# Performance work log

Measured on AMD Instinct MI355X. Metric: run time of the kernel, lower is better.

## Reference

```python
import jax, jax.numpy as jnp
import numpy as np

N_GENE, N_CPG, N_MIRNA = 20000, 60000, 2000
HID, H, NL = 128, 8, 2
C = HID // H
B = 64
NEG_SLOPE = 0.2
LN_EPS = 1e-5
# edge types in HeteroConv order: (src_node_idx, dst_node_idx); node order: 0=gene,1=cpg,2=mirna
EDGE_META = [(1, 0), (0, 1), (2, 0), (0, 2), (0, 0), (0, 0), (1, 1), (2, 2)]


def layernorm(x, g, b):
    mu = jnp.mean(x, axis=-1, keepdims=True)
    var = jnp.mean(jnp.square(x - mu), axis=-1, keepdims=True)
    return (x - mu) * jax.lax.rsqrt(var + LN_EPS) * g + b


def gatv2_conv(x_src, x_dst, ei, Wl, Wr, att, bias):
    """PyG GATv2Conv, add_self_loops=False, concat heads, eval mode (no dropout)."""
    src, dst = ei[0], ei[1]
    n_dst = x_dst.shape[0]
    hs = (x_src @ Wl).reshape(-1, H, C)   # lin_l -> source features [Ns,H,C]
    hd = (x_dst @ Wr).reshape(-1, H, C)   # lin_r -> target features [Nd,H,C]
    e = jax.nn.leaky_relu(hs[src] + hd[dst], NEG_SLOPE)   # [E,H,C]
    logits = jnp.einsum('ehc,hc->eh', e, att)             # [E,H]
    # segment softmax over destination nodes
    m = jax.ops.segment_max(logits, dst, num_segments=n_dst)
    a = jnp.exp(logits - m[dst])
    s = jax.ops.segment_sum(a, dst, num_segments=n_dst)
    alpha = a / (s[dst] + 1e-16)                          # [E,H]
    msg = (hs[src] * alpha[:, :, None]).reshape(-1, HID)  # [E,HID]
    out = jax.ops.segment_sum(msg, dst, num_segments=n_dst)
    return out + bias


def setup_inputs() -> dict:
    key = jax.random.key(0)
    ks = list(jax.random.split(key, 40))
    nk = lambda: ks.pop()
    rn = lambda shape, s=0.05: jax.random.normal(nk(), shape, jnp.float32) * s

    def edges(E, Ns, Nd):
        src = jax.random.randint(nk(), (E,), 0, Ns, jnp.int32)
        dst = jax.random.randint(nk(), (E,), 0, Nd, jnp.int32)
        return jnp.stack([src, dst])

    def self_loops(N):
        ar = jnp.arange(N, dtype=jnp.int32)
        return jnp.stack([ar, ar])

    inp = {
        'batch_gene': rn((B, N_GENE), 1.0),
        'batch_meth': rn((B, N_CPG), 1.0),
        'batch_mirna': rn((B, N_MIRNA), 1.0),
        'emb_gene': rn((N_GENE, HID)),
        'emb_cpg': rn((N_CPG, HID)),
        'emb_mirna': rn((N_MIRNA, HID)),
        'Wl': rn((NL, 8, HID, HID)),
        'Wr': rn((NL, 8, HID, HID)),
        'att': rn((NL, 8, H, C)),
        'bias': rn((NL, 8, HID), 0.01),
        'ln_gamma': jnp.ones((NL, 3, HID), jnp.float32),
        'ln_beta': jnp.zeros((NL, 3, HID), jnp.float32),
        'out_gamma': jnp.ones((3, HID), jnp.float32),
        'out_beta': jnp.zeros((3, HID), jnp.float32),
        'ei_cg': edges(500000, N_CPG, N_GENE),
        'ei_gc': edges(500000, N_GENE, N_CPG),
        'ei_mg': edges(150000, N_MIRNA, N_GENE),
        'ei_gm': edges(150000, N_GENE, N_MIRNA),
        'ei_gg': edges(500000, N_GENE, N_GENE),
        'ei_sg': self_loops(N_GENE),
        'ei_sc': self_loops(N_CPG),
        'ei_sm': self_loops(N_MIRNA),
    }
    return inp


def forward(batch_gene, batch_meth, batch_mirna, emb_gene, emb_cpg, emb_mirna,
            Wl, Wr, att, bias, ln_gamma, ln_beta, out_gamma, out_beta, edge_list):
    x = [emb_gene, emb_cpg, emb_mirna]  # 0=gene,1=cpg,2=mirna
    for l in range(NL):
        agg = [jnp.zeros_like(x[0]), jnp.zeros_like(x[1]), jnp.zeros_like(x[2])]
        for t, (ei, (si, di)) in enumerate(zip(edge_list, EDGE_META)):
            agg[di] = agg[di] + gatv2_conv(x[si], x[di], ei,
                                           Wl[l, t], Wr[l, t], att[l, t], bias[l, t])
        # ELU + residual + LayerNorm per node type (dropout=0 / eval)
        x = [layernorm(x[i] + jax.nn.elu(agg[i]), ln_gamma[l, i], ln_beta[l, i])
             for i in range(3)]
    z_gene = layernorm(batch_gene @ x[0] / np.sqrt(N_GENE), out_gamma[0], out_beta[0])
    z_cpg = layernorm(batch_meth @ x[1] / np.sqrt(N_CPG), out_gamma[1], out_beta[1])
    z_mirna = layernorm(batch_mirna @ x[2] / np.sqrt(N_MIRNA), out_gamma[2], out_beta[2])
    return (z_gene, z_cpg, z_mirna)


def reference(batch_gene, batch_meth, batch_mirna, emb_gene, emb_cpg, emb_mirna,
              Wl, Wr, att, bias, ln_gamma, ln_beta, out_gamma, out_beta,
              ei_cg, ei_gc, ei_mg, ei_gm, ei_gg, ei_sg, ei_sc, ei_sm):
    edge_list = [ei_cg, ei_gc, ei_mg, ei_gm, ei_gg, ei_sg, ei_sc, ei_sm]
    return forward(batch_gene, batch_meth, batch_mirna, emb_gene, emb_cpg, emb_mirna,
                   Wl, Wr, att, bias, ln_gamma, ln_beta, out_gamma, out_beta, edge_list)
```

## Files before the change

### kernel.cpp

```cpp
#include <hip/hip_runtime.h>
#include <math.h>

typedef __attribute__((ext_vector_type(4))) float f32x4;
typedef __attribute__((ext_vector_type(2))) float f32x2;
typedef __attribute__((ext_vector_type(8))) short bf16x8;

__device__ __forceinline__ float b2f(unsigned short u) {
  return __uint_as_float(((unsigned)u) << 16);
}
__device__ __forceinline__ unsigned short f2b(float f) {
  unsigned x = __float_as_uint(f);
  unsigned r = (x + 0x7FFFu + ((x >> 16) & 1u)) >> 16;
  return (unsigned short)r;
}
__device__ __forceinline__ f32x2 bf2x2(unsigned u) {
  f32x2 r;
  r.x = __uint_as_float(u << 16);
  r.y = __uint_as_float(u & 0xFFFF0000u);
  return r;
}
__device__ __forceinline__ f32x2 pk_max(f32x2 a, f32x2 b) {
#if __has_builtin(__builtin_elementwise_max)
  return __builtin_elementwise_max(a, b);
#else
  f32x2 r; r.x = fmaxf(a.x, b.x); r.y = fmaxf(a.y, b.y); return r;
#endif
}
__device__ __forceinline__ f32x2 pk_fma(f32x2 a, f32x2 b, f32x2 c) {
#if __has_builtin(__builtin_elementwise_fma)
  return __builtin_elementwise_fma(a, b, c);
#else
  f32x2 r; r.x = fmaf(a.x, b.x, c.x); r.y = fmaf(a.y, b.y, c.y); return r;
#endif
}

#if __has_builtin(__builtin_amdgcn_cvt_pk_f32_fp8)
template<bool HI>
__device__ __forceinline__ f32x2 fp8x2_dec(unsigned w) {
  return __builtin_amdgcn_cvt_pk_f32_fp8(w, HI);
}
#else
__device__ __forceinline__ float fp8_dec1(unsigned b) {
  unsigned s = b >> 7, e = (b >> 3) & 15, m = b & 7;
  float v = (e == 0) ? (float)m * 0.001953125f
                     : __uint_as_float(((e - 7 + 127) << 23) | (m << 20));
  return s ? -v : v;
}
template<bool HI>
__device__ __forceinline__ f32x2 fp8x2_dec(unsigned w) {
  unsigned h = HI ? (w >> 16) : w;
  f32x2 r; r.x = fp8_dec1(h & 0xFF); r.y = fp8_dec1((h >> 8) & 0xFF);
  return r;
}
#endif
#if __has_builtin(__builtin_amdgcn_cvt_pk_fp8_f32)
__device__ __forceinline__ unsigned char fp8_enc_byte(float a) {
  return (unsigned char)(__builtin_amdgcn_cvt_pk_fp8_f32(a, a, 0, false) & 0xFF);
}
#else
__device__ __forceinline__ unsigned fp8_enc1(float f) {
  unsigned s = (__float_as_uint(f) >> 31) << 7;
  float a = fabsf(f);
  if (a >= 448.f) return s | 0x7E;
  if (a < 0.015625f) {
    int m = (int)(a * 512.f + 0.5f);
    return s | (unsigned)(m > 7 ? 7 : m);
  }
  int ex; (void)frexpf(a, &ex);
  int E = ex - 1;
  float sig = a * exp2f((float)(-E));
  int m = (int)((sig - 1.f) * 8.f + 0.5f);
  if (m == 8) { m = 0; E += 1; }
  if (E > 8) return s | 0x7E;
  return s | (unsigned)((E + 7) << 3) | (unsigned)m;
}
__device__ __forceinline__ unsigned char fp8_enc_byte(float a) {
  return (unsigned char)fp8_enc1(a);
}
#endif

__global__ __launch_bounds__(256) void prep_w(
    const float* __restrict__ Wl, const float* __restrict__ Wr,
    unsigned short* __restrict__ wt)
{
  int elem = blockIdx.x * 256 + threadIdx.x;
  int mat = elem >> 14;
  int c = (elem >> 7) & 127;
  int k = elem & 127;
  const float* srcb = (mat & 1) ? Wr : Wl;
  wt[elem] = f2b(srcb[((long)(mat >> 1) << 14) + (k << 7) + c]);
}

__global__ __launch_bounds__(256) void cast_all(
    const float* __restrict__ e0, const float* __restrict__ e1,
    const float* __restrict__ e2, unsigned short* __restrict__ x0,
    unsigned short* __restrict__ x1, unsigned short* __restrict__ x2,
    int n0, int n1, int n2)
{
  int i = blockIdx.x * 256 + threadIdx.x;
  const float* s; unsigned short* d; int loc = i;
  if (loc < n0) { s = e0; d = x0; }
  else {
    loc -= n0;
    if (loc < n1) { s = e1; d = x1; }
    else { loc -= n1; if (loc >= n2) return; s = e2; d = x2; }
  }
  float4 v = *(const float4*)(s + (long)loc * 4);
  ushort4 o = {f2b(v.x), f2b(v.y), f2b(v.z), f2b(v.w)};
  *(ushort4*)(d + (long)loc * 4) = o;
}

__global__ __launch_bounds__(128) void prep_bias(
    const float* __restrict__ bias, float* __restrict__ bsum)
{
  int c = threadIdx.x;
  const int TM[3] = {0x35, 0x42, 0x88};
  for (int l = 0; l < 2; ++l)
    for (int ty = 0; ty < 3; ++ty) {
      float s = 0.f;
      for (int t = 0; t < 8; ++t)
        if (TM[ty] & (1 << t)) s += bias[(l * 8 + t) * 128 + c];
      bsum[(l * 3 + ty) * 128 + c] = s;
    }
}

struct MPJob {
  const unsigned short* x; int N; int nw;
  const unsigned short* wt[4]; void* out[4]; int mode[4];
};
struct MPArgs { MPJob j[4]; int off[5]; };

__global__ __launch_bounds__(256) void mproj_multi(MPArgs a)
{
  __shared__ __align__(16) char lx[32768];
  __shared__ __align__(16) char lw[32768];
  int blk = blockIdx.x, t = 0;
  while (blk >= a.off[t + 1]) ++t;
  const MPJob& J = a.j[t];
  const long r0 = (long)(blk - a.off[t]) * 128;
  const int tid = threadIdx.x;
  const int N = J.N;

#pragma unroll
  for (int i = 0; i < 8; ++i) {
    int ch = i * 256 + tid;
    int row = ch >> 4, k0 = (ch & 15) << 3;
    uint4 xv = {0u, 0u, 0u, 0u};
    if (r0 + row < N) xv = *(const uint4*)(J.x + (r0 + row) * 128 + k0);
    *(uint4*)(lx + ((row * 256 + k0 * 2) ^ ((row & 7) << 4))) = xv;
  }

  const int lane = tid & 63;
  const int lr = lane & 15, lk = lane >> 4;
  const int rbase = (tid >> 6) * 32;

  for (int w = 0; w < J.nw; ++w) {
    __syncthreads();
    const unsigned short* wt = J.wt[w];
#pragma unroll
    for (int i = 0; i < 8; ++i) {
      int ch = i * 256 + tid;
      int row = ch >> 4;
      uint4 wv = *(const uint4*)(wt + (long)ch * 8);
      *(uint4*)(lw + ((ch * 16) ^ ((row & 7) << 4))) = wv;
    }
    __syncthreads();

    f32x4 acc[2][8] = {};
#pragma unroll
    for (int kb = 0; kb < 4; ++kb) {
      int k = kb * 32 + lk * 8;
      int ra = rbase + lr;
      bf16x8 a0 = *(const bf16x8*)(lx + ((ra * 256 + k * 2) ^ ((ra & 7) << 4)));
      int rb = rbase + 16 + lr;
      bf16x8 a1 = *(const bf16x8*)(lx + ((rb * 256 + k * 2) ^ ((rb & 7) << 4)));
#pragma unroll
      for (int cc = 0; cc < 8; ++cc) {
        int col = cc * 16 + lr;
        bf16x8 bfr = *(const bf16x8*)(lw + ((col * 256 + k * 2) ^ ((col & 7) << 4)));
        acc[0][cc] = __builtin_amdgcn_mfma_f32_16x16x32_bf16(a0, bfr, acc[0][cc], 0, 0, 0);
        acc[1][cc] = __builtin_amdgcn_mfma_f32_16x16x32_bf16(a1, bfr, acc[1][cc], 0, 0, 0);
      }
    }
    int mode = J.mode[w];
    void* outv = J.out[w];
#pragma unroll
    for (int rt = 0; rt < 2; ++rt) {
      int rowb = rbase + rt * 16 + lk * 4;
#pragma unroll
      for (int cc = 0; cc < 8; ++cc) {
        int col = cc * 16 + lr;
#pragma unroll
        for (int q = 0; q < 4; ++q) {
          long row = r0 + rowb + q;
          if (row < N) {
            if (mode == 3)
              ((unsigned char*)outv)[row * 128 + col] = fp8_enc_byte(acc[rt][cc][q]);
            else if (mode == 2)
              ((unsigned short*)outv)[row * 128 + col] = f2b(acc[rt][cc][q]);
            else
              ((float*)outv)[row * 128 + col] = acc[rt][cc][q];
          }
        }
      }
    }
  }
}

struct BArgs {
  const int* src[5]; const int* dst[5];
  int* cnt[5];
  int* tmp[5];
  int* rs[5];
  int* csrc[5];
  int E[5], Nd[5], NB[5], B[5];
  int cOff[6], fOff[6];
};

__global__ __launch_bounds__(256) void bucket_count(BArgs a)
{
  __shared__ int h[512];
  int blk = blockIdx.x, t = 0;
  while (blk >= a.cOff[t + 1]) ++t;
  int lb = blk - a.cOff[t];
  int B = a.B[t], NB = a.NB[t], E = a.E[t];
  for (int i = threadIdx.x; i < B; i += 256) h[i] = 0;
  __syncthreads();
  const int* dst = a.dst[t];
  int base = lb * 4096;
#pragma unroll
  for (int j = 0; j < 16; ++j) {
    int e = base + j * 256 + threadIdx.x;
    if (e < E) atomicAdd(&h[dst[e] >> 7], 1);
  }
  __syncthreads();
  int* cnt = a.cnt[t];
  for (int b = threadIdx.x; b < B; b += 256) cnt[b * NB + lb] = h[b];
}

__global__ __launch_bounds__(1024) void bucket_scan(BArgs a)
{
  int t = blockIdx.x;
  int n = a.B[t] * a.NB[t];
  int* dp = a.cnt[t];
  __shared__ int wsum[16];
  __shared__ int sbase, ctot;
  int tid = threadIdx.x;
  int lane = tid & 63, wid = tid >> 6;
  if (tid == 0) sbase = 0;
  __syncthreads();
  for (int chunk = 0; chunk < n; chunk += 16384) {
    int idx0 = chunk + tid * 16;
    int v[16], lsum = 0;
#pragma unroll
    for (int j = 0; j < 16; ++j) {
      v[j] = (idx0 + j < n) ? dp[idx0 + j] : 0;
      lsum += v[j];
    }
    int sc = lsum;
#pragma unroll
    for (int o = 1; o < 64; o <<= 1) {
      int u = __shfl_up(sc, o);
      if (lane >= o) sc += u;
    }
    if (lane == 63) wsum[wid] = sc;
    __syncthreads();
    if (wid == 0) {
      int w = (lane < 16) ? wsum[lane] : 0;
      int s2 = w;
#pragma unroll
      for (int o = 1; o < 16; o <<= 1) {
        int u = __shfl_up(s2, o);
        if (lane >= o) s2 += u;
      }
      if (lane < 16) wsum[lane] = s2 - w;
      if (lane == 15) ctot = s2;
    }
    __syncthreads();
    int excl = sbase + wsum[wid] + (sc - lsum);
#pragma unroll
    for (int j = 0; j < 16; ++j) {
      if (idx0 + j < n) dp[idx0 + j] = excl;
      excl += v[j];
    }
    __syncthreads();
    if (tid == 0) sbase += ctot;
    __syncthreads();
  }
}

__global__ __launch_bounds__(256) void bucket_scatter(BArgs a)
{
  __shared__ int cur[512];
  int blk = blockIdx.x, t = 0;
  while (blk >= a.cOff[t + 1]) ++t;
  int lb = blk - a.cOff[t];
  int B = a.B[t], NB = a.NB[t], E = a.E[t];
  const int* cnt = a.cnt[t];
  for (int b = threadIdx.x; b < B; b += 256) cur[b] = cnt[b * NB + lb];
  __syncthreads();
  const int* src = a.src[t];
  const int* dst = a.dst[t];
  int* tmp = a.tmp[t];
  int base = lb * 4096;
#pragma unroll
  for (int j = 0; j < 16; ++j) {
    int e = base + j * 256 + threadIdx.x;
    if (e < E) {
      int dv = dst[e];
      int pos = atomicAdd(&cur[dv >> 7], 1);
      tmp[pos] = ((dv & 127) << 16) | src[e];
    }
  }
}

__global__ __launch_bounds__(256) void bucket_finalize(BArgs a)
{
  __shared__ int h[128], sc[128], ex[128], cur[128];
  int blk = blockIdx.x, t = 0;
  while (blk >= a.fOff[t + 1]) ++t;
  int b = blk - a.fOff[t];
  int B = a.B[t], NB = a.NB[t], E = a.E[t], Nd = a.Nd[t];
  const int* cnt = a.cnt[t];
  const int* tmp = a.tmp[t];
  int* rs = a.rs[t];
  int* csrc = a.csrc[t];
  int tid = threadIdx.x;
  int beg = cnt[b * NB];
  int end = (b + 1 < B) ? cnt[(b + 1) * NB] : E;
  if (tid < 128) h[tid] = 0;
  __syncthreads();
  for (int i = beg + tid; i < end; i += 256)
    atomicAdd(&h[tmp[i] >> 16], 1);
  __syncthreads();
  if (tid < 128) sc[tid] = h[tid];
  __syncthreads();
#pragma unroll
  for (int off = 1; off < 128; off <<= 1) {
    int v = (tid < 128 && tid >= off) ? sc[tid - off] : 0;
    __syncthreads();
    if (tid < 128) sc[tid] += v;
    __syncthreads();
  }
  if (tid < 128) {
    ex[tid] = sc[tid] - h[tid];
    cur[tid] = 0;
    int dg = b * 128 + tid;
    if (dg < Nd) rs[dg] = beg + ex[tid];
  }
  if (b == B - 1 && tid == 0) rs[Nd] = E;
  __syncthreads();
  for (int i = beg + tid; i < end; i += 256) {
    int v = tmp[i];
    int d = v >> 16;
    int r = atomicAdd(&cur[d], 1);
    csrc[beg + ex[d] + r] = v & 0xFFFF;
  }
}

struct GSeg {
  const int* rs[3]; const int* csrc[3];
  const unsigned char* hs[3]; const unsigned short* hd[3];
  const float* att[3];
  const float* aggSelf;
  const float* xin;
  float* xf; unsigned short* xb;
  const float* bsum;
  const float* gam; const float* bet;
  int Nd; int ntypes;
};
struct GArgs { GSeg s[3]; int off[4]; };

__global__ __launch_bounds__(256) void gat_gather_ln(GArgs g)
{
  int blk = blockIdx.x, si = 0;
  while (blk >= g.off[si + 1]) ++si;
  const GSeg& sg = g.s[si];
  int d = (blk - g.off[si]) * 4 + (threadIdx.x >> 6);
  if (d >= sg.Nd) return;
  int lane = threadIdx.x & 63;
  int q = lane >> 4, j = lane & 15;
  f32x2 T0 = {0.f, 0.f}, T1 = {0.f, 0.f}, T2 = {0.f, 0.f}, T3 = {0.f, 0.f};
  for (int k = 0; k < sg.ntypes; ++k) {
    const float* ap = sg.att[k] + 8 * j;
    float4 aa = *(const float4*)ap;
    float4 ab = *(const float4*)(ap + 4);
    f32x2 A0 = {aa.x, aa.y}, A1 = {aa.z, aa.w};
    f32x2 A2 = {ab.x, ab.y}, A3 = {ab.z, ab.w};
    uint4 hu = *((const uint4*)(sg.hd[k] + (long)d * 128) + j);
    f32x2 H0 = bf2x2(hu.x), H1 = bf2x2(hu.y);
    f32x2 H2 = bf2x2(hu.z), H3 = bf2x2(hu.w);
    const int* cs = sg.csrc[k];
    const unsigned char* hsk = sg.hs[k];
    int beg = sg.rs[k][d], end = sg.rs[k][d + 1];
    f32x2 n0 = {0.f, 0.f}, n1 = {0.f, 0.f}, n2 = {0.f, 0.f}, n3 = {0.f, 0.f};
    float D = 0.f;

#define GA_EDGE(U)                                                          \
    {                                                                       \
      f32x2 h0 = fp8x2_dec<false>((U).x), h1 = fp8x2_dec<true>((U).x);      \
      f32x2 h2 = fp8x2_dec<false>((U).y), h3 = fp8x2_dec<true>((U).y);      \
      f32x2 v0 = h0 + H0, v1 = h1 + H1, v2 = h2 + H2, v3 = h3 + H3;         \
      v0 = pk_max(v0, v0 * 0.2f);                                           \
      v1 = pk_max(v1, v1 * 0.2f);                                           \
      v2 = pk_max(v2, v2 * 0.2f);                                           \
      v3 = pk_max(v3, v3 * 0.2f);                                           \
      f32x2 pv = pk_fma(v0, A0, pk_fma(v1, A1, pk_fma(v2, A2, v3 * A3)));   \
      float p = pv.x + pv.y;                                                \
      p += __shfl_xor(p, 1);                                                \
      float a = __expf(fminf(p, 60.f));                                     \
      f32x2 av = {a, a};                                                    \
      n0 = pk_fma(h0, av, n0);                                              \
      n1 = pk_fma(h1, av, n1);                                              \
      n2 = pk_fma(h2, av, n2);                                              \
      n3 = pk_fma(h3, av, n3);                                              \
      D += a;                                                               \
    }

    int i = beg + q;
    int sA = (i < end) ? cs[i] : 0;
    int sB = (i + 4 < end) ? cs[i + 4] : 0;
    for (; i + 4 < end; i += 8) {
      uint2 u0 = *((const uint2*)(hsk + (long)sA * 128) + j);
      uint2 u1 = *((const uint2*)(hsk + (long)sB * 128) + j);
      sA = (i + 8 < end) ? cs[i + 8] : 0;
      sB = (i + 12 < end) ? cs[i + 12] : 0;
      GA_EDGE(u0);
      GA_EDGE(u1);
    }
    if (i < end) {
      uint2 u = *((const uint2*)(hsk + (long)sA * 128) + j);
      GA_EDGE(u);
    }
#undef GA_EDGE

#pragma unroll
    for (int o = 16; o < 64; o <<= 1) {
      n0.x += __shfl_xor(n0.x, o); n0.y += __shfl_xor(n0.y, o);
      n1.x += __shfl_xor(n1.x, o); n1.y += __shfl_xor(n1.y, o);
      n2.x += __shfl_xor(n2.x, o); n2.y += __shfl_xor(n2.y, o);
      n3.x += __shfl_xor(n3.x, o); n3.y += __shfl_xor(n3.y, o);
      D += __shfl_xor(D, o);
    }
    float inv = 1.f / (D + 1e-16f);
    f32x2 iv = {inv, inv};
    T0 = pk_fma(n0, iv, T0);
    T1 = pk_fma(n1, iv, T1);
    T2 = pk_fma(n2, iv, T2);
    T3 = pk_fma(n3, iv, T3);
  }

  long base = (long)d * 128 + 8 * j;
  float4 sA0 = *(const float4*)(sg.aggSelf + base);
  float4 sA1 = *(const float4*)(sg.aggSelf + base + 4);
  float4 bb0 = *(const float4*)(sg.bsum + 8 * j);
  float4 bb1 = *(const float4*)(sg.bsum + 8 * j + 4);
  float v[8];
  v[0] = sA0.x + T0.x + bb0.x; v[1] = sA0.y + T0.y + bb0.y;
  v[2] = sA0.z + T1.x + bb0.z; v[3] = sA0.w + T1.y + bb0.w;
  v[4] = sA1.x + T2.x + bb1.x; v[5] = sA1.y + T2.y + bb1.y;
  v[6] = sA1.z + T3.x + bb1.z; v[7] = sA1.w + T3.y + bb1.w;
#pragma unroll
  for (int c = 0; c < 8; ++c) v[c] = v[c] > 0.f ? v[c] : __expf(v[c]) - 1.f;
  float4 xi0 = *(const float4*)(sg.xin + base);
  float4 xi1 = *(const float4*)(sg.xin + base + 4);
  float xr[8] = {xi0.x + v[0], xi0.y + v[1], xi0.z + v[2], xi0.w + v[3],
                 xi1.x + v[4], xi1.y + v[5], xi1.z + v[6], xi1.w + v[7]};
  float ssum = ((xr[0] + xr[1]) + (xr[2] + xr[3])) +
               ((xr[4] + xr[5]) + (xr[6] + xr[7]));
#pragma unroll
  for (int o = 1; o < 16; o <<= 1) ssum += __shfl_xor(ssum, o);
  float mu = ssum * 0.0078125f;
  float qs = 0.f;
#pragma unroll
  for (int c = 0; c < 8; ++c) { float dd = xr[c] - mu; qs += dd * dd; }
#pragma unroll
  for (int o = 1; o < 16; o <<= 1) qs += __shfl_xor(qs, o);
  float rr = rsqrtf(qs * 0.0078125f + 1e-5f);
  float4 g0 = *(const float4*)(sg.gam + 8 * j);
  float4 g1 = *(const float4*)(sg.gam + 8 * j + 4);
  float4 e0 = *(const float4*)(sg.bet + 8 * j);
  float4 e1 = *(const float4*)(sg.bet + 8 * j + 4);
  float y[8];
  y[0] = (xr[0] - mu) * rr * g0.x + e0.x;
  y[1] = (xr[1] - mu) * rr * g0.y + e0.y;
  y[2] = (xr[2] - mu) * rr * g0.z + e0.z;
  y[3] = (xr[3] - mu) * rr * g0.w + e0.w;
  y[4] = (xr[4] - mu) * rr * g1.x + e1.x;
  y[5] = (xr[5] - mu) * rr * g1.y + e1.y;
  y[6] = (xr[6] - mu) * rr * g1.z + e1.z;
  y[7] = (xr[7] - mu) * rr * g1.w + e1.w;
  if (q == 0) {
    float4 o0 = {y[0], y[1], y[2], y[3]};
    float4 o1 = {y[4], y[5], y[6], y[7]};
    *(float4*)(sg.xf + base) = o0;
    *(float4*)(sg.xf + base + 4) = o1;
    uint4 ub;
    ub.x = (unsigned)f2b(y[0]) | ((unsigned)f2b(y[1]) << 16);
    ub.y = (unsigned)f2b(y[2]) | ((unsigned)f2b(y[3]) << 16);
    ub.z = (unsigned)f2b(y[4]) | ((unsigned)f2b(y[5]) << 16);
    ub.w = (unsigned)f2b(y[6]) | ((unsigned)f2b(y[7]) << 16);
    *(uint4*)(sg.xb + base) = ub;
  }
}

struct ZArgs {
  const float* batch[3]; const float* x[3]; float* zp[3]; int N[3];
  int off[4];
};

__global__ __launch_bounds__(256) void zgemm_all(ZArgs z)
{
  __shared__ __align__(16) float xl[64 * 128];
  __shared__ __align__(16) float bl[64 * 65];
  int blk = blockIdx.x, s = 0;
  while (blk >= z.off[s + 1]) ++s;
  int chunk = blk - z.off[s];
  const float* batch = z.batch[s];
  const float* x = z.x[s];
  int N = z.N[s];
  int tid = threadIdx.x;
  int n0 = chunk * 64;
  for (int i = tid; i < 64 * 128; i += 256) {
    int nn = i >> 7;
    xl[i] = (n0 + nn < N) ? x[(long)(n0 + nn) * 128 + (i & 127)] : 0.f;
  }
  for (int i = tid; i < 64 * 64; i += 256) {
    int b = i >> 6, nn = i & 63;
    bl[nn * 65 + b] = (n0 + nn < N) ? batch[(long)b * N + n0 + nn] : 0.f;
  }
  __syncthreads();
  int cg = (tid & 31) * 4;
  int bg = (tid >> 5) * 8;
  float acc[8][4] = {};
  for (int nn = 0; nn < 64; ++nn) {
    float4 xv = *(const float4*)(xl + nn * 128 + cg);
#pragma unroll
    for (int i = 0; i < 8; ++i) {
      float bv = bl[nn * 65 + bg + i];
      acc[i][0] = fmaf(bv, xv.x, acc[i][0]);
      acc[i][1] = fmaf(bv, xv.y, acc[i][1]);
      acc[i][2] = fmaf(bv, xv.z, acc[i][2]);
      acc[i][3] = fmaf(bv, xv.w, acc[i][3]);
    }
  }
  float* zp = z.zp[s] + (long)chunk * 8192;
#pragma unroll
  for (int i = 0; i < 8; ++i) {
    float4 v = {acc[i][0], acc[i][1], acc[i][2], acc[i][3]};
    *(float4*)(zp + (bg + i) * 128 + cg) = v;
  }
}

__global__ __launch_bounds__(256) void zfinal(
    const float* __restrict__ zp0, const float* __restrict__ zp1,
    const float* __restrict__ zp2, int G0, int G1, int G2,
    float s0, float s1, float s2, const float* __restrict__ gam,
    const float* __restrict__ bet, float* __restrict__ out)
{
  int blk = blockIdx.x;
  int ty = blk >> 4;
  int rowL = (blk & 15) * 4 + (threadIdx.x >> 6);
  int lane = threadIdx.x & 63;
  const float* zp = ty == 0 ? zp0 : (ty == 1 ? zp1 : zp2);
  int G = ty == 0 ? G0 : (ty == 1 ? G1 : G2);
  float sc = ty == 0 ? s0 : (ty == 1 ? s1 : s2);
  long i0 = rowL * 128 + lane, i1 = i0 + 64;
  float a0[8], a1[8];
#pragma unroll
  for (int u = 0; u < 8; ++u) { a0[u] = 0.f; a1[u] = 0.f; }
  int g = 0;
  for (; g + 8 <= G; g += 8) {
#pragma unroll
    for (int u = 0; u < 8; ++u) {
      a0[u] += zp[(long)(g + u) * 8192 + i0];
      a1[u] += zp[(long)(g + u) * 8192 + i1];
    }
  }
  for (; g < G; ++g) { a0[0] += zp[(long)g * 8192 + i0]; a1[0] += zp[(long)g * 8192 + i1]; }
  float x0 = (((a0[0] + a0[1]) + (a0[2] + a0[3])) + ((a0[4] + a0[5]) + (a0[6] + a0[7]))) * sc;
  float x1 = (((a1[0] + a1[1]) + (a1[2] + a1[3])) + ((a1[4] + a1[5]) + (a1[6] + a1[7]))) * sc;
  float s = x0 + x1;
#pragma unroll
  for (int o = 32; o > 0; o >>= 1) s += __shfl_xor(s, o);
  float mu = s * 0.0078125f;
  float d0 = x0 - mu, d1 = x1 - mu;
  float qv = d0 * d0 + d1 * d1;
#pragma unroll
  for (int o = 32; o > 0; o >>= 1) qv += __shfl_xor(qv, o);
  float r = rsqrtf(qv * 0.0078125f + 1e-5f);
  long base = (long)(ty * 64 + rowL) * 128;
  out[base + lane]      = d0 * r * gam[ty * 128 + lane]      + bet[ty * 128 + lane];
  out[base + 64 + lane] = d1 * r * gam[ty * 128 + 64 + lane] + bet[ty * 128 + 64 + lane];
}

extern "C" void kernel_launch(void* const* d_in, const int* in_sizes, int n_in,
                              void* d_out, int out_size, void* d_ws, size_t ws_size,
                              hipStream_t stream)
{
  const float* batchp[3] = {(const float*)d_in[0], (const float*)d_in[1],
                            (const float*)d_in[2]};
  const float* emb[3] = {(const float*)d_in[3], (const float*)d_in[4],
                         (const float*)d_in[5]};
  const float* Wl   = (const float*)d_in[6];
  const float* Wr   = (const float*)d_in[7];
  const float* att  = (const float*)d_in[8];
  const float* bias = (const float*)d_in[9];
  const float* lng  = (const float*)d_in[10];
  const float* lnb  = (const float*)d_in[11];
  const float* outg = (const float*)d_in[12];
  const float* outb = (const float*)d_in[13];
  const int* eiP[8]; int E[8];
  for (int t = 0; t < 8; ++t) { eiP[t] = (const int*)d_in[14 + t]; E[t] = in_sizes[14 + t] / 2; }
  int Nn[3] = {in_sizes[3] / 128, in_sizes[4] / 128, in_sizes[5] / 128};
  long Ntot = (long)Nn[0] + Nn[1] + Nn[2];

  const int SI[5] = {1, 0, 2, 0, 0};
  const int DI[5] = {0, 1, 0, 2, 0};

  char* p = (char*)d_ws;
  auto carve = [&](size_t b) -> void* {
    void* r = (void*)p; p += (b + 255) & ~(size_t)255; return r;
  };
  float* xf[3];
  for (int ty = 0; ty < 3; ++ty) xf[ty] = (float*)carve((size_t)Nn[ty] * 128 * 4);
  unsigned short* xb[3];
  for (int ty = 0; ty < 3; ++ty) xb[ty] = (unsigned short*)carve((size_t)Nn[ty] * 128 * 2);
  float* aggAll = (float*)carve((size_t)Ntot * 128 * 4);
  float* agg[3] = {aggAll, aggAll + (long)Nn[0] * 128, aggAll + ((long)Nn[0] + Nn[1]) * 128};
  unsigned short* hdT[5];
  for (int t = 0; t < 5; ++t) hdT[t] = (unsigned short*)carve((size_t)Nn[DI[t]] * 128 * 2);
  long hsElems = 0;
  for (int t = 0; t < 5; ++t) hsElems += (long)Nn[SI[t]] * 128;
  unsigned char* hs8base = (unsigned char*)carve((size_t)hsElems);
  unsigned char* hs8T[5];
  {
    unsigned char* q8 = hs8base;
    for (int t = 0; t < 5; ++t) { hs8T[t] = q8; q8 += (long)Nn[SI[t]] * 128; }
  }
  float* bsumBuf = (float*)carve(2 * 3 * 128 * 4);
  unsigned short* wtb = (unsigned short*)carve((size_t)32 * 16384 * 2);

  int nch[3];
  for (int ty = 0; ty < 3; ++ty) nch[ty] = (Nn[ty] + 63) / 64;
  float* zpBase = (float*)carve((size_t)(nch[0] + nch[1] + nch[2]) * 8192 * 4);
  float* zp[3];
  zp[0] = zpBase;
  zp[1] = zp[0] + (long)nch[0] * 8192;
  zp[2] = zp[1] + (long)nch[1] * 8192;

  BArgs ba;
  {
    int cOff = 0, fOff = 0;
    for (int t = 0; t < 5; ++t) {
      int nd = Nn[DI[t]];
      ba.src[t] = eiP[t];
      ba.dst[t] = eiP[t] + E[t];
      ba.E[t] = E[t];
      ba.Nd[t] = nd;
      ba.NB[t] = (E[t] + 4095) / 4096;
      ba.B[t] = (nd + 127) / 128;
      ba.cnt[t] = (int*)carve((size_t)ba.B[t] * ba.NB[t] * 4);
      ba.tmp[t] = (int*)carve((size_t)E[t] * 4);
      ba.rs[t] = (int*)carve((size_t)(nd + 1) * 4);
      ba.csrc[t] = (int*)carve((size_t)E[t] * 4);
      ba.cOff[t] = cOff; cOff += ba.NB[t];
      ba.fOff[t] = fOff; fOff += ba.B[t];
    }
    ba.cOff[5] = cOff;
    ba.fOff[5] = fOff;
  }
  if ((size_t)(p - (char*)d_ws) > ws_size) return;

  auto WTB = [&](int l, int t, int which) {
    return wtb + ((long)((l * 8 + t) * 2 + which) << 14);
  };

  prep_w<<<2048, 256, 0, stream>>>(Wl, Wr, wtb);
  {
    int n0 = Nn[0] * 32, n1 = Nn[1] * 32, n2 = Nn[2] * 32;
    cast_all<<<(int)((n0 + n1 + n2 + 255) / 256), 256, 0, stream>>>(
        emb[0], emb[1], emb[2], xb[0], xb[1], xb[2], n0, n1, n2);
  }
  prep_bias<<<1, 128, 0, stream>>>(bias, bsumBuf);

  bucket_count<<<ba.cOff[5], 256, 0, stream>>>(ba);
  bucket_scan<<<5, 1024, 0, stream>>>(ba);
  bucket_scatter<<<ba.cOff[5], 256, 0, stream>>>(ba);
  bucket_finalize<<<ba.fOff[5], 256, 0, stream>>>(ba);

  const int GT[3][3] = {{0, 2, 4}, {1, -1, -1}, {3, -1, -1}};
  const int GN[3] = {3, 1, 1};

  for (int l = 0; l < 2; ++l) {
    const float* xinf[3] = {l == 0 ? emb[0] : xf[0],
                            l == 0 ? emb[1] : xf[1],
                            l == 0 ? emb[2] : xf[2]};
    MPArgs mp;
    {
      int off = 0, nj = 0;
      auto addJob = [&](const unsigned short* x, int N) {
        mp.j[nj].x = x; mp.j[nj].N = N; mp.j[nj].nw = 0;
        mp.off[nj] = off; off += (N + 127) / 128;
        return nj++;
      };
      auto addW = [&](int ji, const unsigned short* wt, void* out, int mode) {
        MPJob& J = mp.j[ji];
        J.wt[J.nw] = wt; J.out[J.nw] = out; J.mode[J.nw] = mode; J.nw++;
      };
      int ga_ = addJob(xb[0], Nn[0]);
      addW(ga_, WTB(l, 1, 0), hs8T[1], 3);
      addW(ga_, WTB(l, 3, 0), hs8T[3], 3);
      addW(ga_, WTB(l, 4, 0), hs8T[4], 3);
      addW(ga_, WTB(l, 0, 1), hdT[0], 2);
      int gb_ = addJob(xb[0], Nn[0]);
      addW(gb_, WTB(l, 2, 1), hdT[2], 2);
      addW(gb_, WTB(l, 4, 1), hdT[4], 2);
      addW(gb_, WTB(l, 5, 0), agg[0], 0);
      int cj_ = addJob(xb[1], Nn[1]);
      addW(cj_, WTB(l, 0, 0), hs8T[0], 3);
      addW(cj_, WTB(l, 1, 1), hdT[1], 2);
      addW(cj_, WTB(l, 6, 0), agg[1], 0);
      int mj_ = addJob(xb[2], Nn[2]);
      addW(mj_, WTB(l, 2, 0), hs8T[2], 3);
      addW(mj_, WTB(l, 3, 1), hdT[3], 2);
      addW(mj_, WTB(l, 7, 0), agg[2], 0);
      mp.off[4] = off;
      mproj_multi<<<off, 256, 0, stream>>>(mp);
    }
    GArgs ga;
    {
      int off = 0;
      for (int s = 0; s < 3; ++s) {
        GSeg& sg = ga.s[s];
        sg.aggSelf = agg[s];
        sg.xin = xinf[s];
        sg.xf = xf[s];
        sg.xb = xb[s];
        sg.bsum = bsumBuf + (long)(l * 3 + s) * 128;
        sg.gam = lng + (long)(l * 3 + s) * 128;
        sg.bet = lnb + (long)(l * 3 + s) * 128;
        sg.Nd = Nn[s];
        sg.ntypes = GN[s];
        for (int k = 0; k < GN[s]; ++k) {
          int t = GT[s][k];
          sg.rs[k] = ba.rs[t];
          sg.csrc[k] = ba.csrc[t];
          sg.hs[k] = hs8T[t];
          sg.hd[k] = hdT[t];
          sg.att[k] = att + (long)(l * 8 + t) * 128;
        }
        ga.off[s] = off;
        off += (Nn[s] + 3) / 4;
      }
      ga.off[3] = off;
      gat_gather_ln<<<off, 256, 0, stream>>>(ga);
    }
  }

  ZArgs za;
  {
    int off = 0;
    for (int ty = 0; ty < 3; ++ty) {
      za.batch[ty] = batchp[ty];
      za.x[ty] = xf[ty];
      za.zp[ty] = zp[ty];
      za.N[ty] = Nn[ty];
      za.off[ty] = off;
      off += nch[ty];
    }
    za.off[3] = off;
    zgemm_all<<<off, 256, 0, stream>>>(za);
  }
  zfinal<<<48, 256, 0, stream>>>(
      zp[0], zp[1], zp[2], nch[0], nch[1], nch[2],
      (float)(1.0 / sqrt((double)Nn[0])), (float)(1.0 / sqrt((double)Nn[1])),
      (float)(1.0 / sqrt((double)Nn[2])), outg, outb, (float*)d_out);
}
```

Measured before the change: 554.3 us.

## Map one 16-lane group per CpG node in gather and halve z-GEMM partials

Result: faster. 473.3 us, median of 2 (-14.6%).

```diff
diff --git a/kernel.cpp b/kernel.cpp
--- a/kernel.cpp
+++ b/kernel.cpp
@@ -367,34 +367,9 @@
   float* xf; unsigned short* xb;
   const float* bsum;
   const float* gam; const float* bet;
-  int Nd; int ntypes;
+  int Nd; int ntypes; int fast;
 };
 struct GArgs { GSeg s[3]; int off[4]; };
-
-__global__ __launch_bounds__(256) void gat_gather_ln(GArgs g)
-{
-  int blk = blockIdx.x, si = 0;
-  while (blk >= g.off[si + 1]) ++si;
-  const GSeg& sg = g.s[si];
-  int d = (blk - g.off[si]) * 4 + (threadIdx.x >> 6);
-  if (d >= sg.Nd) return;
-  int lane = threadIdx.x & 63;
-  int q = lane >> 4, j = lane & 15;
-  f32x2 T0 = {0.f, 0.f}, T1 = {0.f, 0.f}, T2 = {0.f, 0.f}, T3 = {0.f, 0.f};
-  for (int k = 0; k < sg.ntypes; ++k) {
-    const float* ap = sg.att[k] + 8 * j;
-    float4 aa = *(const float4*)ap;
-    float4 ab = *(const float4*)(ap + 4);
-    f32x2 A0 = {aa.x, aa.y}, A1 = {aa.z, aa.w};
-    f32x2 A2 = {ab.x, ab.y}, A3 = {ab.z, ab.w};
-    uint4 hu = *((const uint4*)(sg.hd[k] + (long)d * 128) + j);
-    f32x2 H0 = bf2x2(hu.x), H1 = bf2x2(hu.y);
-    f32x2 H2 = bf2x2(hu.z), H3 = bf2x2(hu.w);
-    const int* cs = sg.csrc[k];
-    const unsigned char* hsk = sg.hs[k];
-    int beg = sg.rs[k][d], end = sg.rs[k][d + 1];
-    f32x2 n0 = {0.f, 0.f}, n1 = {0.f, 0.f}, n2 = {0.f, 0.f}, n3 = {0.f, 0.f};
-    float D = 0.f;
 
 #define GA_EDGE(U)                                                          \
     {                                                                       \
@@ -417,6 +392,133 @@
       D += a;                                                               \
     }
 
+__global__ __launch_bounds__(256) void gat_gather_ln(GArgs g)
+{
+  int blk = blockIdx.x, si = 0;
+  while (blk >= g.off[si + 1]) ++si;
+  const GSeg& sg = g.s[si];
+  int lane = threadIdx.x & 63;
+
+  if (sg.fast) {
+    int wv = threadIdx.x >> 6;
+    int grp = lane >> 4, j = lane & 15;
+    int d = (blk - g.off[si]) * 16 + wv * 4 + grp;
+    bool act = d < sg.Nd;
+    const float* ap = sg.att[0] + 8 * j;
+    float4 aa = *(const float4*)ap;
+    float4 ab = *(const float4*)(ap + 4);
+    f32x2 A0 = {aa.x, aa.y}, A1 = {aa.z, aa.w};
+    f32x2 A2 = {ab.x, ab.y}, A3 = {ab.z, ab.w};
+    f32x2 H0 = {0.f, 0.f}, H1 = {0.f, 0.f}, H2 = {0.f, 0.f}, H3 = {0.f, 0.f};
+    int beg = 0, end = 0;
+    if (act) {
+      uint4 hu = *((const uint4*)(sg.hd[0] + (long)d * 128) + j);
+      H0 = bf2x2(hu.x); H1 = bf2x2(hu.y);
+      H2 = bf2x2(hu.z); H3 = bf2x2(hu.w);
+      beg = sg.rs[0][d];
+      end = sg.rs[0][d + 1];
+    }
+    const int* cs = sg.csrc[0];
+    const unsigned char* hsk = sg.hs[0];
+    f32x2 n0 = {0.f, 0.f}, n1 = {0.f, 0.f}, n2 = {0.f, 0.f}, n3 = {0.f, 0.f};
+    float D = 0.f;
+    int i = beg;
+    int sA = (i < end) ? cs[i] : 0;
+    int sB = (i + 1 < end) ? cs[i + 1] : 0;
+    for (; i + 1 < end; i += 2) {
+      uint2 u0 = *((const uint2*)(hsk + (long)sA * 128) + j);
+      uint2 u1 = *((const uint2*)(hsk + (long)sB * 128) + j);
+      sA = (i + 2 < end) ? cs[i + 2] : 0;
+      sB = (i + 3 < end) ? cs[i + 3] : 0;
+      GA_EDGE(u0);
+      GA_EDGE(u1);
+    }
+    if (i < end) {
+      uint2 u = *((const uint2*)(hsk + (long)sA * 128) + j);
+      GA_EDGE(u);
+    }
+    float inv = 1.f / (D + 1e-16f);
+    f32x2 iv = {inv, inv};
+    f32x2 T0 = n0 * iv, T1 = n1 * iv, T2 = n2 * iv, T3 = n3 * iv;
+
+    long base = (long)d * 128 + 8 * j;
+    float v[8] = {T0.x, T0.y, T1.x, T1.y, T2.x, T2.y, T3.x, T3.y};
+    if (act) {
+      float4 sA0 = *(const float4*)(sg.aggSelf + base);
+      float4 sA1 = *(const float4*)(sg.aggSelf + base + 4);
+      float4 bb0 = *(const float4*)(sg.bsum + 8 * j);
+      float4 bb1 = *(const float4*)(sg.bsum + 8 * j + 4);
+      v[0] += sA0.x + bb0.x; v[1] += sA0.y + bb0.y;
+      v[2] += sA0.z + bb0.z; v[3] += sA0.w + bb0.w;
+      v[4] += sA1.x + bb1.x; v[5] += sA1.y + bb1.y;
+      v[6] += sA1.z + bb1.z; v[7] += sA1.w + bb1.w;
+    }
+#pragma unroll
+    for (int c = 0; c < 8; ++c) v[c] = v[c] > 0.f ? v[c] : __expf(v[c]) - 1.f;
+    float xr[8] = {v[0], v[1], v[2], v[3], v[4], v[5], v[6], v[7]};
+    if (act) {
+      float4 xi0 = *(const float4*)(sg.xin + base);
+      float4 xi1 = *(const float4*)(sg.xin + base + 4);
+      xr[0] += xi0.x; xr[1] += xi0.y; xr[2] += xi0.z; xr[3] += xi0.w;
+      xr[4] += xi1.x; xr[5] += xi1.y; xr[6] += xi1.z; xr[7] += xi1.w;
+    }
+    float ssum = ((xr[0] + xr[1]) + (xr[2] + xr[3])) +
+                 ((xr[4] + xr[5]) + (xr[6] + xr[7]));
+#pragma unroll
+    for (int o = 1; o < 16; o <<= 1) ssum += __shfl_xor(ssum, o);
+    float mu = ssum * 0.0078125f;
+    float qs = 0.f;
+#pragma unroll
+    for (int c = 0; c < 8; ++c) { float dd = xr[c] - mu; qs += dd * dd; }
+#pragma unroll
+    for (int o = 1; o < 16; o <<= 1) qs += __shfl_xor(qs, o);
+    float rr = rsqrtf(qs * 0.0078125f + 1e-5f);
+    if (act) {
+      float4 g0 = *(const float4*)(sg.gam + 8 * j);
+      float4 g1 = *(const float4*)(sg.gam + 8 * j + 4);
+      float4 e0 = *(const float4*)(sg.bet + 8 * j);
+      float4 e1 = *(const float4*)(sg.bet + 8 * j + 4);
+      float y[8];
+      y[0] = (xr[0] - mu) * rr * g0.x + e0.x;
+      y[1] = (xr[1] - mu) * rr * g0.y + e0.y;
+      y[2] = (xr[2] - mu) * rr * g0.z + e0.z;
+      y[3] = (xr[3] - mu) * rr * g0.w + e0.w;
+      y[4] = (xr[4] - mu) * rr * g1.x + e1.x;
+      y[5] = (xr[5] - mu) * rr * g1.y + e1.y;
+      y[6] = (xr[6] - mu) * rr * g1.z + e1.z;
+      y[7] = (xr[7] - mu) * rr * g1.w + e1.w;
+      float4 o0 = {y[0], y[1], y[2], y[3]};
+      float4 o1 = {y[4], y[5], y[6], y[7]};
+      *(float4*)(sg.xf + base) = o0;
+      *(float4*)(sg.xf + base + 4) = o1;
+      uint4 ub;
+      ub.x = (unsigned)f2b(y[0]) | ((unsigned)f2b(y[1]) << 16);
+      ub.y = (unsigned)f2b(y[2]) | ((unsigned)f2b(y[3]) << 16);
+      ub.z = (unsigned)f2b(y[4]) | ((unsigned)f2b(y[5]) << 16);
+      ub.w = (unsigned)f2b(y[6]) | ((unsigned)f2b(y[7]) << 16);
+      *(uint4*)(sg.xb + base) = ub;
+    }
+    return;
+  }
+
+  int d = (blk - g.off[si]) * 4 + (threadIdx.x >> 6);
+  if (d >= sg.Nd) return;
+  int q = lane >> 4, j = lane & 15;
+  f32x2 T0 = {0.f, 0.f}, T1 = {0.f, 0.f}, T2 = {0.f, 0.f}, T3 = {0.f, 0.f};
+  for (int k = 0; k < sg.ntypes; ++k) {
+    const float* ap = sg.att[k] + 8 * j;
+    float4 aa = *(const float4*)ap;
+    float4 ab = *(const float4*)(ap + 4);
+    f32x2 A0 = {aa.x, aa.y}, A1 = {aa.z, aa.w};
+    f32x2 A2 = {ab.x, ab.y}, A3 = {ab.z, ab.w};
+    uint4 hu = *((const uint4*)(sg.hd[k] + (long)d * 128) + j);
+    f32x2 H0 = bf2x2(hu.x), H1 = bf2x2(hu.y);
+    f32x2 H2 = bf2x2(hu.z), H3 = bf2x2(hu.w);
+    const int* cs = sg.csrc[k];
+    const unsigned char* hsk = sg.hs[k];
+    int beg = sg.rs[k][d], end = sg.rs[k][d + 1];
+    f32x2 n0 = {0.f, 0.f}, n1 = {0.f, 0.f}, n2 = {0.f, 0.f}, n3 = {0.f, 0.f};
+    float D = 0.f;
     int i = beg + q;
     int sA = (i < end) ? cs[i] : 0;
     int sB = (i + 4 < end) ? cs[i + 4] : 0;
@@ -432,8 +534,6 @@
       uint2 u = *((const uint2*)(hsk + (long)sA * 128) + j);
       GA_EDGE(u);
     }
-#undef GA_EDGE
-
 #pragma unroll
     for (int o = 16; o < 64; o <<= 1) {
       n0.x += __shfl_xor(n0.x, o); n0.y += __shfl_xor(n0.y, o);
@@ -503,6 +603,7 @@
     *(uint4*)(sg.xb + base) = ub;
   }
 }
+#undef GA_EDGE
 
 struct ZArgs {
   const float* batch[3]; const float* x[3]; float* zp[3]; int N[3];
@@ -515,36 +616,41 @@
   __shared__ __align__(16) float bl[64 * 65];
   int blk = blockIdx.x, s = 0;
   while (blk >= z.off[s + 1]) ++s;
-  int chunk = blk - z.off[s];
+  int c = blk - z.off[s];
   const float* batch = z.batch[s];
   const float* x = z.x[s];
   int N = z.N[s];
   int tid = threadIdx.x;
-  int n0 = chunk * 64;
-  for (int i = tid; i < 64 * 128; i += 256) {
-    int nn = i >> 7;
-    xl[i] = (n0 + nn < N) ? x[(long)(n0 + nn) * 128 + (i & 127)] : 0.f;
-  }
-  for (int i = tid; i < 64 * 64; i += 256) {
-    int b = i >> 6, nn = i & 63;
-    bl[nn * 65 + b] = (n0 + nn < N) ? batch[(long)b * N + n0 + nn] : 0.f;
-  }
-  __syncthreads();
   int cg = (tid & 31) * 4;
   int bg = (tid >> 5) * 8;
   float acc[8][4] = {};
-  for (int nn = 0; nn < 64; ++nn) {
-    float4 xv = *(const float4*)(xl + nn * 128 + cg);
-#pragma unroll
-    for (int i = 0; i < 8; ++i) {
-      float bv = bl[nn * 65 + bg + i];
-      acc[i][0] = fmaf(bv, xv.x, acc[i][0]);
-      acc[i][1] = fmaf(bv, xv.y, acc[i][1]);
-      acc[i][2] = fmaf(bv, xv.z, acc[i][2]);
-      acc[i][3] = fmaf(bv, xv.w, acc[i][3]);
-    }
-  }
-  float* zp = z.zp[s] + (long)chunk * 8192;
+#pragma unroll
+  for (int cc = 0; cc < 2; ++cc) {
+    int n0 = (c * 2 + cc) * 64;
+    if (n0 >= N) break;
+    __syncthreads();
+    for (int i = tid; i < 64 * 128; i += 256) {
+      int nn = i >> 7;
+      xl[i] = (n0 + nn < N) ? x[(long)(n0 + nn) * 128 + (i & 127)] : 0.f;
+    }
+    for (int i = tid; i < 64 * 64; i += 256) {
+      int b = i >> 6, nn = i & 63;
+      bl[nn * 65 + b] = (n0 + nn < N) ? batch[(long)b * N + n0 + nn] : 0.f;
+    }
+    __syncthreads();
+    for (int nn = 0; nn < 64; ++nn) {
+      float4 xv = *(const float4*)(xl + nn * 128 + cg);
+#pragma unroll
+      for (int i = 0; i < 8; ++i) {
+        float bv = bl[nn * 65 + bg + i];
+        acc[i][0] = fmaf(bv, xv.x, acc[i][0]);
+        acc[i][1] = fmaf(bv, xv.y, acc[i][1]);
+        acc[i][2] = fmaf(bv, xv.z, acc[i][2]);
+        acc[i][3] = fmaf(bv, xv.w, acc[i][3]);
+      }
+    }
+  }
+  float* zp = z.zp[s] + (long)c * 8192;
 #pragma unroll
   for (int i = 0; i < 8; ++i) {
     float4 v = {acc[i][0], acc[i][1], acc[i][2], acc[i][3]};
@@ -641,13 +747,16 @@
   float* bsumBuf = (float*)carve(2 * 3 * 128 * 4);
   unsigned short* wtb = (unsigned short*)carve((size_t)32 * 16384 * 2);
 
-  int nch[3];
-  for (int ty = 0; ty < 3; ++ty) nch[ty] = (Nn[ty] + 63) / 64;
-  float* zpBase = (float*)carve((size_t)(nch[0] + nch[1] + nch[2]) * 8192 * 4);
+  int nch[3], nch2[3];
+  for (int ty = 0; ty < 3; ++ty) {
+    nch[ty] = (Nn[ty] + 63) / 64;
+    nch2[ty] = (nch[ty] + 1) / 2;
+  }
+  float* zpBase = (float*)carve((size_t)(nch2[0] + nch2[1] + nch2[2]) * 8192 * 4);
   float* zp[3];
   zp[0] = zpBase;
-  zp[1] = zp[0] + (long)nch[0] * 8192;
-  zp[2] = zp[1] + (long)nch[1] * 8192;
+  zp[1] = zp[0] + (long)nch2[0] * 8192;
+  zp[2] = zp[1] + (long)nch2[1] * 8192;
 
   BArgs ba;
   {
@@ -742,6 +851,7 @@
         sg.bet = lnb + (long)(l * 3 + s) * 128;
         sg.Nd = Nn[s];
         sg.ntypes = GN[s];
+        sg.fast = (s == 1) ? 1 : 0;
         for (int k = 0; k < GN[s]; ++k) {
           int t = GT[s][k];
           sg.rs[k] = ba.rs[t];
@@ -751,7 +861,7 @@
           sg.att[k] = att + (long)(l * 8 + t) * 128;
         }
         ga.off[s] = off;
-        off += (Nn[s] + 3) / 4;
+        off += sg.fast ? (Nn[s] + 15) / 16 : (Nn[s] + 3) / 4;
       }
       ga.off[3] = off;
       gat_gather_ln<<<off, 256, 0, stream>>>(ga);
@@ -767,13 +877,13 @@
       za.zp[ty] = zp[ty];
       za.N[ty] = Nn[ty];
       za.off[ty] = off;
-      off += nch[ty];
+      off += nch2[ty];
     }
     za.off[3] = off;
     zgemm_all<<<off, 256, 0, stream>>>(za);
   }
   zfinal<<<48, 256, 0, stream>>>(
-      zp[0], zp[1], zp[2], nch[0], nch[1], nch[2],
+      zp[0], zp[1], zp[2], nch2[0], nch2[1], nch2[2],
       (float)(1.0 / sqrt((double)Nn[0])), (float)(1.0 / sqrt((double)Nn[1])),
       (float)(1.0 / sqrt((double)Nn[2])), outg, outb, (float*)d_out);
 }
```
